# Kernel tuning notes

Measured on AMD Instinct MI355X. Metric: run time of the kernel, lower is better.

Reference implementation:

```python
import jax, jax.numpy as jnp
import numpy as np

N_NODES = 20000
N_EDGES = 640000
HIDDEN = 128
NUM_FILTERS = 128
NUM_RBF = 50
NUM_LAYERS = 6
MAX_Z = 100
CUTOFF_UPPER = 5.0
CUTOFF_LOWER = 0.0


def _cosine_cutoff(d):
    # torchmd CosineCutoff with cutoff_lower == 0
    c = 0.5 * (jnp.cos(d * jnp.pi / CUTOFF_UPPER) + 1.0)
    return c * (d < CUTOFF_UPPER).astype(d.dtype)


def setup_inputs() -> dict:
    key = jax.random.key(0)
    ks = jax.random.split(key, 16)
    s = 0.05
    z = jax.random.randint(ks[0], (N_NODES,), 0, MAX_Z)
    pos = jax.random.uniform(ks[1], (N_NODES, 3), dtype=jnp.float32) * 3.0
    src = jax.random.randint(ks[2], (N_EDGES,), 0, N_NODES)
    off = jax.random.randint(ks[3], (N_EDGES,), 1, N_NODES)
    dst = (src + off) % N_NODES  # no self loops -> d > 0 a.s.
    edge_index = jnp.stack([src, dst])
    batch = jnp.zeros((N_NODES,), dtype=jnp.int32)
    # expnorm RBF initial params (ExpNormalSmearing._initial_params)
    start = float(np.exp(-CUTOFF_UPPER + CUTOFF_LOWER))
    rbf_means = jnp.linspace(start, 1.0, NUM_RBF, dtype=jnp.float32)
    rbf_betas = jnp.full((NUM_RBF,), (2.0 / NUM_RBF * (1.0 - start)) ** -2, dtype=jnp.float32)

    def w(k, shape):
        return jax.random.normal(k, shape, dtype=jnp.float32) * s

    L = NUM_LAYERS
    return dict(
        z=z, pos=pos, edge_index=edge_index, batch=batch,
        emb_table=w(ks[4], (MAX_Z, HIDDEN)),
        nbr_emb_table=w(ks[5], (MAX_Z, HIDDEN)),
        nbr_proj_W=w(ks[6], (NUM_RBF, HIDDEN)),
        nbr_proj_b=jnp.zeros((HIDDEN,), jnp.float32),
        combine_W=w(ks[7], (2 * HIDDEN, HIDDEN)),
        combine_b=jnp.zeros((HIDDEN,), jnp.float32),
        rbf_means=rbf_means, rbf_betas=rbf_betas,
        mlp_W1=w(ks[8], (L, NUM_RBF, NUM_FILTERS)),
        mlp_b1=jnp.zeros((L, NUM_FILTERS), jnp.float32),
        mlp_W2=w(ks[9], (L, NUM_FILTERS, NUM_FILTERS)),
        mlp_b2=jnp.zeros((L, NUM_FILTERS), jnp.float32),
        lin1_W=w(ks[10], (L, HIDDEN, NUM_FILTERS)),
        lin2_W=w(ks[11], (L, NUM_FILTERS, HIDDEN)),
        lin2_b=jnp.zeros((L, HIDDEN), jnp.float32),
        lin_W=w(ks[12], (L, HIDDEN, HIDDEN)),
        lin_b=jnp.zeros((L, HIDDEN), jnp.float32),
    )


def reference(z, pos, edge_index, batch, emb_table, nbr_emb_table,
              nbr_proj_W, nbr_proj_b, combine_W, combine_b,
              rbf_means, rbf_betas,
              mlp_W1, mlp_b1, mlp_W2, mlp_b2,
              lin1_W, lin2_W, lin2_b, lin_W, lin_b):
    src, dst = edge_index[0], edge_index[1]
    # Distance (loop=False): edge_vec = pos[src] - pos[dst]
    vec = pos[src] - pos[dst]                      # [E, 3]
    d = jnp.sqrt(jnp.sum(vec * vec, axis=-1))      # [E]
    C = _cosine_cutoff(d)                          # [E]
    alpha = 5.0 / (CUTOFF_UPPER - CUTOFF_LOWER)
    # ExpNormalSmearing: C(d) * exp(-beta * (exp(alpha*(-d+low)) - mu)^2)
    edge_attr = C[:, None] * jnp.exp(
        -rbf_betas * (jnp.exp(alpha * (-d[:, None] + CUTOFF_LOWER)) - rbf_means) ** 2
    )                                              # [E, R]
    x = emb_table[z]                               # [N, H]
    # NeighborEmbedding (self-loop edges masked out, add aggregation)
    nl_mask = (src != dst).astype(x.dtype)
    Wn = (edge_attr @ nbr_proj_W + nbr_proj_b) * (C * nl_mask)[:, None]  # [E, H]
    xn = nbr_emb_table[z]
    agg = jax.ops.segment_sum(xn[src] * Wn, dst, num_segments=N_NODES)
    x = jnp.concatenate([x, agg], axis=1) @ combine_W + combine_b

    def layer(xc, p):
        W1, b1, W2, b2, l1W, l2W, l2b, lW, lb = p
        # CFConv filter: MLP(edge_attr) * cosine_cutoff
        Wf = (jax.nn.silu(edge_attr @ W1 + b1) @ W2 + b2) * C[:, None]   # [E, F]
        h = xc @ l1W                                                      # [N, F]
        ag = jax.ops.segment_sum(h[src] * Wf, dst, num_segments=N_NODES)  # scatter-add
        h = jax.nn.silu(ag @ l2W + l2b)
        h = h @ lW + lb
        return xc + h, None

    x, _ = jax.lax.scan(layer, x, (mlp_W1, mlp_b1, mlp_W2, mlp_b2,
                                   lin1_W, lin2_W, lin2_b, lin_W, lin_b))
    return x
```

## Files before the change

### kernel.cpp

```cpp
#include <hip/hip_runtime.h>
#include <hip/hip_bf16.h>
#include <math.h>

#define NN 20000
#define NE 640000
#define H  128
#define RB 50
#define NL 6
#define TBINS 4096

typedef unsigned short u16;
typedef __attribute__((ext_vector_type(8))) short short8v;
typedef __attribute__((ext_vector_type(4))) float f32x4;

__device__ __forceinline__ u16 f2b(float v) {
  unsigned x = __float_as_uint(v);
  unsigned r = (x + 0x7FFFu + ((x >> 16) & 1u)) >> 16;
  return (u16)r;
}
__device__ __forceinline__ float b2f(u16 u) {
  return __uint_as_float(((unsigned int)u) << 16);
}

__global__ void k_zero_i32(int* __restrict__ p, int n) {
  int i = blockIdx.x * blockDim.x + threadIdx.x;
  if (i < n) p[i] = 0;
}
__global__ void k_hist(const int* __restrict__ ei, int* __restrict__ counts) {
  int e = blockIdx.x * blockDim.x + threadIdx.x;
  if (e < NE) atomicAdd(&counts[ei[NE + e]], 1);
}
__global__ __launch_bounds__(1024) void k_scan(const int* __restrict__ counts,
                                               int* __restrict__ cursor) {
  __shared__ int tsum[1024];
  int tid = threadIdx.x;
  int base = tid * 20;
  int s = 0;
  #pragma unroll
  for (int j = 0; j < 20; ++j) {
    int i = base + j;
    s += (i < NN) ? counts[i] : 0;
  }
  tsum[tid] = s;
  __syncthreads();
  for (int off = 1; off < 1024; off <<= 1) {
    int t = (tid >= off) ? tsum[tid - off] : 0;
    __syncthreads();
    tsum[tid] += t;
    __syncthreads();
  }
  int run = (tid > 0) ? tsum[tid - 1] : 0;
  #pragma unroll
  for (int j = 0; j < 20; ++j) {
    int i = base + j;
    if (i < NN) { cursor[i] = run; run += counts[i]; }
  }
}
__global__ void k_place(const int* __restrict__ ei, int* __restrict__ cursor,
                        int* __restrict__ perm) {
  int e = blockIdx.x * blockDim.x + threadIdx.x;
  if (e < NE) {
    int d = ei[NE + e];
    int p = atomicAdd(&cursor[d], 1);
    perm[p] = e;
  }
}

__global__ void k_edge(const int* __restrict__ ei, const int* __restrict__ perm,
                       const float* __restrict__ pos,
                       int* __restrict__ srcS, float* __restrict__ tvS) {
  int p = blockIdx.x * 256 + threadIdx.x;
  if (p >= NE) return;
  int e = perm[p];
  int s = ei[e], t = ei[NE + e];
  srcS[p] = s;
  float dx = pos[3*s]   - pos[3*t];
  float dy = pos[3*s+1] - pos[3*t+1];
  float dz = pos[3*s+2] - pos[3*t+2];
  float d = sqrtf(dx*dx + dy*dy + dz*dz);
  tvS[p] = expf(-d);
}

__global__ __launch_bounds__(256) void k_tbuild(
    const float* __restrict__ means, const float* __restrict__ betas,
    const float* __restrict__ npW, const float* __restrict__ npb,
    const float* __restrict__ W1, const float* __restrict__ b1,
    const float* __restrict__ W2, const float* __restrict__ b2,
    u16* __restrict__ tb)
{
  int t  = blockIdx.x / (TBINS / 32);
  int j0 = (blockIdx.x % (TBINS / 32)) * 32;
  __shared__ float sAttr[32][52];
  __shared__ float sCut[32];
  __shared__ float sT[32][132];
  int tid = threadIdx.x;
  float tv0 = expf(-5.f);
  float dtv = (1.f - tv0) / (float)(TBINS - 1);
  for (int idx = tid; idx < 32 * RB; idx += 256) {
    int r = idx / RB, k = idx % RB;
    float tv = tv0 + (j0 + r) * dtv;
    float d = -logf(tv);
    float C = 0.5f * (cosf(d * 0.628318530717958647692f) + 1.f);
    if (d >= 5.f) C = 0.f;
    float diff = tv - means[k];
    sAttr[r][k] = C * expf(-betas[k] * diff * diff);
    if (k == 0) sCut[r] = C;
  }
  __syncthreads();
  int g = tid >> 5, c0 = (tid & 31) * 4, eb = g * 4;
  float acc[4][4];
  #pragma unroll
  for (int i = 0; i < 4; ++i)
    for (int j = 0; j < 4; ++j) acc[i][j] = 0.f;
  const float* Wa = (t == 0) ? npW : (W1 + (size_t)(t - 1) * RB * H);
  for (int k = 0; k < RB; ++k) {
    float4 wv = *(const float4*)&Wa[(size_t)k * H + c0];
    #pragma unroll
    for (int i = 0; i < 4; ++i) {
      float a = sAttr[eb + i][k];
      acc[i][0] += a * wv.x; acc[i][1] += a * wv.y;
      acc[i][2] += a * wv.z; acc[i][3] += a * wv.w;
    }
  }
  size_t obase = (size_t)t * TBINS * H;
  int pb = (c0 & 15) * 8 + (c0 >> 4);
  if (t == 0) {
    float4 b4 = *(const float4*)&npb[c0];
    float bvA[4] = {b4.x, b4.y, b4.z, b4.w};
    #pragma unroll
    for (int i = 0; i < 4; ++i) {
      float Cv = sCut[eb + i];
      size_t rb = obase + (size_t)(j0 + eb + i) * H;
      #pragma unroll
      for (int j = 0; j < 4; ++j)
        tb[rb + pb + 8 * j] = f2b((acc[i][j] + bvA[j]) * Cv);
    }
  } else {
    float4 b4 = *(const float4*)&b1[(size_t)(t - 1) * H + c0];
    float bvA[4] = {b4.x, b4.y, b4.z, b4.w};
    #pragma unroll
    for (int i = 0; i < 4; ++i) {
      #pragma unroll
      for (int j = 0; j < 4; ++j) {
        float v = acc[i][j] + bvA[j];
        sT[eb + i][c0 + j] = v / (1.f + __expf(-v));
      }
    }
    __syncthreads();
    #pragma unroll
    for (int i = 0; i < 4; ++i)
      for (int j = 0; j < 4; ++j) acc[i][j] = 0.f;
    const float* Wb = W2 + (size_t)(t - 1) * H * H;
    for (int k = 0; k < H; ++k) {
      float4 wv = *(const float4*)&Wb[(size_t)k * H + c0];
      #pragma unroll
      for (int i = 0; i < 4; ++i) {
        float a = sT[eb + i][k];
        acc[i][0] += a * wv.x; acc[i][1] += a * wv.y;
        acc[i][2] += a * wv.z; acc[i][3] += a * wv.w;
      }
    }
    float4 b24 = *(const float4*)&b2[(size_t)(t - 1) * H + c0];
    float bvB[4] = {b24.x, b24.y, b24.z, b24.w};
    #pragma unroll
    for (int i = 0; i < 4; ++i) {
      float Cv = sCut[eb + i];
      size_t rb = obase + (size_t)(j0 + eb + i) * H;
      #pragma unroll
      for (int j = 0; j < 4; ++j)
        tb[rb + pb + 8 * j] = f2b((acc[i][j] + bvB[j]) * Cv);
    }
  }
}

#define WBLK (128 * 136)
__global__ void k_prepw2(const float* __restrict__ l2W, const float* __restrict__ lW,
                         const float* __restrict__ l1W, const float* __restrict__ cW,
                         u16* __restrict__ wt) {
  int i = blockIdx.x * 256 + threadIdx.x;
  if (i >= (3 * NL + 2) * WBLK) return;
  if (i < 3 * NL * WBLK) {
    int a = i / (NL * WBLK);
    int r = i % (NL * WBLK);
    int l = r / WBLK;
    int r2 = r % WBLK;
    int n = r2 / 136, k = r2 % 136;
    const float* src = (a == 0) ? l2W : (a == 1) ? lW : l1W;
    wt[i] = (k < H) ? f2b(src[(size_t)l * H * H + (size_t)k * H + n]) : (u16)0;
  } else {
    int j = i - 3 * NL * WBLK;
    int which = j / WBLK;
    int r2 = j % WBLK;
    int n = r2 / 136, k = r2 % 136;
    wt[i] = (k < H) ? f2b(cW[(size_t)(which * 128 + k) * H + n]) : (u16)0;
  }
}

__global__ void k_embed(const int* __restrict__ z, const float* __restrict__ emb,
                        const float* __restrict__ nemb,
                        float* __restrict__ x, u16* __restrict__ xnb) {
  int i = blockIdx.x * blockDim.x + threadIdx.x;
  if (i >= NN * H) return;
  int n = i >> 7, c = i & (H - 1);
  long o = (long)z[n] * H + c;
  x[i] = emb[o];
  xnb[(size_t)n * H + ((c & 15) * 8 + (c >> 4))] = f2b(nemb[o]);
}

__global__ __launch_bounds__(256) void k_eso(
    const int* __restrict__ counts, const int* __restrict__ cursor,
    const int* __restrict__ srcS, const float* __restrict__ tvS,
    const u16* __restrict__ tb, const u16* __restrict__ hsrc,
    float* __restrict__ agg, int maskSelf)
{
  int tid = threadIdx.x;
  int n = blockIdx.x * 16 + (tid >> 4);
  int r16 = tid & 15;
  int cnt = counts[n];
  long e0 = (long)cursor[n] - cnt;
  float tv0 = expf(-5.f);
  float inv = (float)(TBINS - 1) / (1.f - tv0);
  float vsum[8];
  #pragma unroll
  for (int ct = 0; ct < 8; ++ct) vsum[ct] = 0.f;
  int P0_s = 0, P1_s = 0, P2_s = 0;
  float P0_w = 0.f, P1_w = 0.f, P2_w = 0.f;
  short8v P0_hv, P0_lo, P0_hi, P1_hv, P1_lo, P1_hi, P2_hv, P2_lo, P2_hi;
#define ISSUE(P, ii) { int _i = (ii); if (_i < cnt) { \
    long e = e0 + _i; \
    P##_s = srcS[e]; float tvv = tvS[e]; \
    P##_hv = *(const short8v*)&hsrc[(size_t)P##_s * H + r16 * 8]; \
    float u = fminf(fmaxf((tvv - tv0) * inv, 0.f), (float)(TBINS - 1) - 1e-3f); \
    int jj = (int)u; P##_w = u - (float)jj; \
    P##_lo = *(const short8v*)&tb[(size_t)jj * H + r16 * 8]; \
    P##_hi = *(const short8v*)&tb[(size_t)(jj + 1) * H + r16 * 8]; } }
#define CONSUME(P) { \
    float m = (maskSelf && P##_s == n) ? 0.f : 1.f; \
    _Pragma("unroll") \
    for (int ct = 0; ct < 8; ++ct) { \
      float lo = b2f((u16)P##_lo[ct]); \
      float hi = b2f((u16)P##_hi[ct]); \
      vsum[ct] += (lo + P##_w * (hi - lo)) * m * b2f((u16)P##_hv[ct]); \
    } }
  ISSUE(P0, 0); ISSUE(P1, 1); ISSUE(P2, 2);
  for (int i = 0; i < cnt; i += 3) {
    CONSUME(P0); ISSUE(P0, i + 3);
    if (i + 1 < cnt) { CONSUME(P1); ISSUE(P1, i + 4); }
    if (i + 2 < cnt) { CONSUME(P2); ISSUE(P2, i + 5); }
  }
#undef ISSUE
#undef CONSUME
  float* ap = agg + (size_t)n * H + r16;
  #pragma unroll
  for (int ct = 0; ct < 8; ++ct) ap[ct * 16] = vsum[ct];
}

__global__ __launch_bounds__(256) void k_combineM(
    const float* __restrict__ xb, const float* __restrict__ ag,
    const u16* __restrict__ cWt0, const u16* __restrict__ cWt1,
    const float* __restrict__ cb, const u16* __restrict__ l1W0t,
    float* __restrict__ xout, u16* __restrict__ hb)
{
  __shared__ __align__(16) u16 sX[64 * 136];
  __shared__ __align__(16) u16 sG[64 * 136];
  int tid = threadIdx.x;
  int lane = tid & 63, wv = tid >> 6;
  int r16 = lane & 15, g4 = lane >> 4;
  int n0 = blockIdx.x * 64;
  #pragma unroll
  for (int j = 0; j < 8; ++j) {
    int f4 = tid + j * 256;
    int r = f4 >> 5, c4 = f4 & 31;
    int n = n0 + r;
    float4 vx = make_float4(0.f, 0.f, 0.f, 0.f);
    float4 vg = make_float4(0.f, 0.f, 0.f, 0.f);
    if (n < NN) {
      vx = *(const float4*)&xb[(size_t)n * H + c4 * 4];
      vg = *(const float4*)&ag[(size_t)n * H + c4 * 4];
    }
    *(unsigned*)&sX[r * 136 + c4 * 4]     = (unsigned)f2b(vx.x) | ((unsigned)f2b(vx.y) << 16);
    *(unsigned*)&sX[r * 136 + c4 * 4 + 2] = (unsigned)f2b(vx.z) | ((unsigned)f2b(vx.w) << 16);
    *(unsigned*)&sG[r * 136 + c4 * 4]     = (unsigned)f2b(vg.x) | ((unsigned)f2b(vg.y) << 16);
    *(unsigned*)&sG[r * 136 + c4 * 4 + 2] = (unsigned)f2b(vg.z) | ((unsigned)f2b(vg.w) << 16);
  }
  __syncthreads();
  int wrow = wv * 16;
  f32x4 acc[8];
  #pragma unroll
  for (int ct = 0; ct < 8; ++ct) acc[ct] = (f32x4){0.f, 0.f, 0.f, 0.f};
  #pragma unroll
  for (int kt = 0; kt < 4; ++kt) {
    short8v aF = *(const short8v*)&sX[(wrow + r16) * 136 + kt * 32 + g4 * 8];
    #pragma unroll
    for (int ct = 0; ct < 8; ++ct) {
      short8v bF = *(const short8v*)&cWt0[(ct * 16 + r16) * 136 + kt * 32 + g4 * 8];
      acc[ct] = __builtin_amdgcn_mfma_f32_16x16x32_bf16(aF, bF, acc[ct], 0, 0, 0);
    }
  }
  #pragma unroll
  for (int kt = 0; kt < 4; ++kt) {
    short8v aF = *(const short8v*)&sG[(wrow + r16) * 136 + kt * 32 + g4 * 8];
    #pragma unroll
    for (int ct = 0; ct < 8; ++ct) {
      short8v bF = *(const short8v*)&cWt1[(ct * 16 + r16) * 136 + kt * 32 + g4 * 8];
      acc[ct] = __builtin_amdgcn_mfma_f32_16x16x32_bf16(aF, bF, acc[ct], 0, 0, 0);
    }
  }
  #pragma unroll
  for (int ct = 0; ct < 8; ++ct) {
    float bb = cb[ct * 16 + r16];
    #pragma unroll
    for (int r = 0; r < 4; ++r) {
      int n = n0 + wrow + g4 * 4 + r;
      if (n < NN) {
        float o = acc[ct][r] + bb;
        xout[(size_t)n * H + ct * 16 + r16] = o;
        sX[(wrow + g4 * 4 + r) * 136 + ct * 16 + r16] = f2b(o);
      }
    }
  }
  #pragma unroll
  for (int ct = 0; ct < 8; ++ct) acc[ct] = (f32x4){0.f, 0.f, 0.f, 0.f};
  #pragma unroll
  for (int kt = 0; kt < 4; ++kt) {
    short8v aF = *(const short8v*)&sX[(wrow + r16) * 136 + kt * 32 + g4 * 8];
    #pragma unroll
    for (int ct = 0; ct < 8; ++ct) {
      short8v bF = *(const short8v*)&l1W0t[(ct * 16 + r16) * 136 + kt * 32 + g4 * 8];
      acc[ct] = __builtin_amdgcn_mfma_f32_16x16x32_bf16(aF, bF, acc[ct], 0, 0, 0);
    }
  }
  #pragma unroll
  for (int r = 0; r < 4; ++r) {
    int n = n0 + wrow + g4 * 4 + r;
    if (n < NN) {
      short8v hv;
      #pragma unroll
      for (int ct = 0; ct < 8; ++ct) hv[ct] = (short)f2b(acc[ct][r]);
      *(short8v*)&hb[(size_t)n * H + r16 * 8] = hv;
    }
  }
}

__global__ __launch_bounds__(256) void k_gemmM(
    const float* __restrict__ A, const u16* __restrict__ W2t, const float* __restrict__ b2,
    const u16* __restrict__ W3t, const float* __restrict__ b3,
    const float* __restrict__ xin, float* __restrict__ xout,
    const u16* __restrict__ l1Wnt, u16* __restrict__ hb)
{
  __shared__ __align__(16) u16 sA[64 * 136];
  __shared__ __align__(16) u16 sT[64 * 136];
  int tid = threadIdx.x;
  int lane = tid & 63, wv = tid >> 6;
  int r16 = lane & 15, g4 = lane >> 4;
  int n0 = blockIdx.x * 64;
  #pragma unroll
  for (int j = 0; j < 8; ++j) {
    int f4 = tid + j * 256;
    int r = f4 >> 5, c4 = f4 & 31;
    int n = n0 + r;
    float4 v = make_float4(0.f, 0.f, 0.f, 0.f);
    if (n < NN) v = *(const float4*)&A[(size_t)n * H + c4 * 4];
    *(unsigned*)&sA[r * 136 + c4 * 4]     = (unsigned)f2b(v.x) | ((unsigned)f2b(v.y) << 16);
    *(unsigned*)&sA[r * 136 + c4 * 4 + 2] = (unsigned)f2b(v.z) | ((unsigned)f2b(v.w) << 16);
  }
  __syncthreads();
  int wrow = wv * 16;
  f32x4 acc[8];
  #pragma unroll
  for (int ct = 0; ct < 8; ++ct) acc[ct] = (f32x4){0.f, 0.f, 0.f, 0.f};
  #pragma unroll
  for (int kt = 0; kt < 4; ++kt) {
    short8v aF = *(const short8v*)&sA[(wrow + r16) * 136 + kt * 32 + g4 * 8];
    #pragma unroll
    for (int ct = 0; ct < 8; ++ct) {
      short8v bF = *(const short8v*)&W2t[(ct * 16 + r16) * 136 + kt * 32 + g4 * 8];
      acc[ct] = __builtin_amdgcn_mfma_f32_16x16x32_bf16(aF, bF, acc[ct], 0, 0, 0);
    }
  }
  #pragma unroll
  for (int ct = 0; ct < 8; ++ct) {
    float bb = b2[ct * 16 + r16];
    #pragma unroll
    for (int r = 0; r < 4; ++r) {
      float v = acc[ct][r] + bb;
      v = v / (1.f + __expf(-v));
      sT[(wrow + g4 * 4 + r) * 136 + ct * 16 + r16] = f2b(v);
    }
  }
  #pragma unroll
  for (int ct = 0; ct < 8; ++ct) acc[ct] = (f32x4){0.f, 0.f, 0.f, 0.f};
  #pragma unroll
  for (int kt = 0; kt < 4; ++kt) {
    short8v aF = *(const short8v*)&sT[(wrow + r16) * 136 + kt * 32 + g4 * 8];
    #pragma unroll
    for (int ct = 0; ct < 8; ++ct) {
      short8v bF = *(const short8v*)&W3t[(ct * 16 + r16) * 136 + kt * 32 + g4 * 8];
      acc[ct] = __builtin_amdgcn_mfma_f32_16x16x32_bf16(aF, bF, acc[ct], 0, 0, 0);
    }
  }
  #pragma unroll
  for (int ct = 0; ct < 8; ++ct) {
    float bb = b3[ct * 16 + r16];
    #pragma unroll
    for (int r = 0; r < 4; ++r) {
      int n = n0 + wrow + g4 * 4 + r;
      if (n < NN) {
        float o = acc[ct][r] + bb + xin[(size_t)n * H + ct * 16 + r16];
        xout[(size_t)n * H + ct * 16 + r16] = o;
        sA[(wrow + g4 * 4 + r) * 136 + ct * 16 + r16] = f2b(o);
      }
    }
  }
  if (!l1Wnt) return;
  #pragma unroll
  for (int ct = 0; ct < 8; ++ct) acc[ct] = (f32x4){0.f, 0.f, 0.f, 0.f};
  #pragma unroll
  for (int kt = 0; kt < 4; ++kt) {
    short8v aF = *(const short8v*)&sA[(wrow + r16) * 136 + kt * 32 + g4 * 8];
    #pragma unroll
    for (int ct = 0; ct < 8; ++ct) {
      short8v bF = *(const short8v*)&l1Wnt[(ct * 16 + r16) * 136 + kt * 32 + g4 * 8];
      acc[ct] = __builtin_amdgcn_mfma_f32_16x16x32_bf16(aF, bF, acc[ct], 0, 0, 0);
    }
  }
  #pragma unroll
  for (int r = 0; r < 4; ++r) {
    int n = n0 + wrow + g4 * 4 + r;
    if (n < NN) {
      short8v hv;
      #pragma unroll
      for (int ct = 0; ct < 8; ++ct) hv[ct] = (short)f2b(acc[ct][r]);
      *(short8v*)&hb[(size_t)n * H + r16 * 8] = hv;
    }
  }
}

extern "C" void kernel_launch(void* const* d_in, const int* in_sizes, int n_in,
                              void* d_out, int out_size, void* d_ws, size_t ws_size,
                              hipStream_t stream) {
  int bo = (n_in >= 4 && in_sizes[3] == NN) ? 0 : -1;
  const int*   z     = (const int*)d_in[0];
  const float* pos   = (const float*)d_in[1];
  const int*   ei    = (const int*)d_in[2];
  const float* emb   = (const float*)d_in[4 + bo];
  const float* nemb  = (const float*)d_in[5 + bo];
  const float* npW   = (const float*)d_in[6 + bo];
  const float* npb   = (const float*)d_in[7 + bo];
  const float* cW    = (const float*)d_in[8 + bo];
  const float* cb    = (const float*)d_in[9 + bo];
  const float* means = (const float*)d_in[10 + bo];
  const float* betas = (const float*)d_in[11 + bo];
  const float* W1    = (const float*)d_in[12 + bo];
  const float* b1    = (const float*)d_in[13 + bo];
  const float* W2    = (const float*)d_in[14 + bo];
  const float* b2    = (const float*)d_in[15 + bo];
  const float* l1W   = (const float*)d_in[16 + bo];
  const float* l2W   = (const float*)d_in[17 + bo];
  const float* l2b   = (const float*)d_in[18 + bo];
  const float* lW    = (const float*)d_in[19 + bo];
  const float* lb    = (const float*)d_in[20 + bo];

  char* w = (char*)d_ws;
  auto alloc = [&](size_t bytes) { char* p = w; w += (bytes + 255) & ~(size_t)255; return p; };
  int*   counts = (int*)  alloc((size_t)NN * 4);
  int*   cursor = (int*)  alloc((size_t)NN * 4);
  int*   perm   = (int*)  alloc((size_t)NE * 4);
  int*   srcS   = (int*)  alloc((size_t)NE * 4);
  float* tvS    = (float*)alloc((size_t)NE * 4);
  u16*   tb     = (u16*)  alloc((size_t)7 * TBINS * H * 2);
  u16*   wt     = (u16*)  alloc((size_t)(3 * NL + 2) * WBLK * 2);
  float* xbuf   = (float*)alloc((size_t)NN * H * 4);
  float* agg    = (float*)alloc((size_t)NN * H * 4);
  u16*   xnb    = (u16*)  alloc((size_t)NN * H * 2);
  u16*   hbuf   = (u16*)  alloc((size_t)NN * H * 2);

  u16* l2Wt = wt;
  u16* lWt  = wt + (size_t)NL * WBLK;
  u16* l1Wt = wt + (size_t)2 * NL * WBLK;
  u16* cWt0 = wt + (size_t)3 * NL * WBLK;
  u16* cWt1 = cWt0 + WBLK;

  dim3 b256(256);
  int gE256 = (NE + 255) / 256;
  int gNH   = (NN * H + 255) / 256;
  int gESO  = NN / 16;
  int gM    = (NN + 63) / 64;
  int gTB   = 7 * (TBINS / 32);
  int gPW   = ((3 * NL + 2) * WBLK + 255) / 256;

  k_zero_i32<<<(NN + 255) / 256, b256, 0, stream>>>(counts, NN);
  k_hist<<<gE256, b256, 0, stream>>>(ei, counts);
  k_scan<<<1, 1024, 0, stream>>>(counts, cursor);
  k_place<<<gE256, b256, 0, stream>>>(ei, cursor, perm);
  k_edge<<<gE256, b256, 0, stream>>>(ei, perm, pos, srcS, tvS);
  k_tbuild<<<gTB, b256, 0, stream>>>(means, betas, npW, npb, W1, b1, W2, b2, tb);
  k_prepw2<<<gPW, b256, 0, stream>>>(l2W, lW, l1W, cW, wt);
  k_embed<<<gNH, b256, 0, stream>>>(z, emb, nemb, xbuf, xnb);

  k_eso<<<gESO, b256, 0, stream>>>(counts, cursor, srcS, tvS, tb, xnb, agg, 1);
  k_combineM<<<gM, b256, 0, stream>>>(xbuf, agg, cWt0, cWt1, cb, l1Wt, xbuf, hbuf);

  for (int l = 0; l < NL; ++l) {
    k_eso<<<gESO, b256, 0, stream>>>(counts, cursor, srcS, tvS,
                                     tb + (size_t)(1 + l) * TBINS * H,
                                     hbuf, agg, 0);
    const u16* l1Wnt = (l + 1 < NL) ? (l1Wt + (size_t)(l + 1) * WBLK) : nullptr;
    float* xo = (l == NL - 1) ? (float*)d_out : xbuf;
    k_gemmM<<<gM, b256, 0, stream>>>(agg, l2Wt + (size_t)l * WBLK, l2b + (size_t)l * H,
                                     lWt + (size_t)l * WBLK, lb + (size_t)l * H,
                                     xbuf, xo, l1Wnt, hbuf);
  }
}
```

Baseline: 674.9 us.

## Fuse edge gather-aggregation into per-layer node GEMM kernels with ping-pong h buffers

The separate edge aggregation kernel is merged into the node MLP kernels, for both the embedding-combine stage and every interaction layer. Each 64-node block now walks its own nodes' edges, writing bf16 aggregates straight into shared memory. This removes the fp32 agg buffer's global write and read-back, plus one launch per layer. Because other blocks may still be reading h while a block writes the next layer's h, h now alternates between two buffers. The cost is much less gather parallelism: about 313 blocks, with each 16-thread group walking 4 nodes one after another, which may hurt latency hiding in the memory-bound gather.

Result: slower. 1.001 ms (+48.3%).

```diff
diff --git a/kernel.cpp b/kernel.cpp
--- a/kernel.cpp
+++ b/kernel.cpp
@@ -8,6 +8,7 @@
 #define RB 50
 #define NL 6
 #define TBINS 4096
+#define WBLK (128 * 136)
 
 typedef unsigned short u16;
 typedef __attribute__((ext_vector_type(8))) short short8v;
@@ -173,7 +174,6 @@
   }
 }
 
-#define WBLK (128 * 136)
 __global__ void k_prepw2(const float* __restrict__ l2W, const float* __restrict__ lW,
                          const float* __restrict__ l1W, const float* __restrict__ cW,
                          u16* __restrict__ wt) {
@@ -207,22 +207,17 @@
   xnb[(size_t)n * H + ((c & 15) * 8 + (c >> 4))] = f2b(nemb[o]);
 }
 
-__global__ __launch_bounds__(256) void k_eso(
-    const int* __restrict__ counts, const int* __restrict__ cursor,
+__device__ __forceinline__ void edge_walk(
+    int n, int r16, const int* __restrict__ counts, const int* __restrict__ cursor,
     const int* __restrict__ srcS, const float* __restrict__ tvS,
     const u16* __restrict__ tb, const u16* __restrict__ hsrc,
-    float* __restrict__ agg, int maskSelf)
+    int maskSelf, float tv0, float inv, float vsum[8])
 {
-  int tid = threadIdx.x;
-  int n = blockIdx.x * 16 + (tid >> 4);
-  int r16 = tid & 15;
+  #pragma unroll
+  for (int ct = 0; ct < 8; ++ct) vsum[ct] = 0.f;
+  if (n >= NN) return;
   int cnt = counts[n];
   long e0 = (long)cursor[n] - cnt;
-  float tv0 = expf(-5.f);
-  float inv = (float)(TBINS - 1) / (1.f - tv0);
-  float vsum[8];
-  #pragma unroll
-  for (int ct = 0; ct < 8; ++ct) vsum[ct] = 0.f;
   int P0_s = 0, P1_s = 0, P2_s = 0;
   float P0_w = 0.f, P1_w = 0.f, P2_w = 0.f;
   short8v P0_hv, P0_lo, P0_hi, P1_hv, P1_lo, P1_hi, P2_hv, P2_lo, P2_hi;
@@ -250,13 +245,112 @@
   }
 #undef ISSUE
 #undef CONSUME
-  float* ap = agg + (size_t)n * H + r16;
-  #pragma unroll
-  for (int ct = 0; ct < 8; ++ct) ap[ct * 16] = vsum[ct];
-}
-
-__global__ __launch_bounds__(256) void k_combineM(
-    const float* __restrict__ xb, const float* __restrict__ ag,
+}
+
+__global__ __launch_bounds__(256) void k_fused(
+    const int* __restrict__ counts, const int* __restrict__ cursor,
+    const int* __restrict__ srcS, const float* __restrict__ tvS,
+    const u16* __restrict__ tb, const u16* __restrict__ hsrc,
+    const u16* __restrict__ W2t, const float* __restrict__ b2,
+    const u16* __restrict__ W3t, const float* __restrict__ b3,
+    const float* __restrict__ xin, float* __restrict__ xout,
+    const u16* __restrict__ l1Wnt, u16* __restrict__ hb)
+{
+  __shared__ __align__(16) u16 sA[64 * 136];
+  __shared__ __align__(16) u16 sT[64 * 136];
+  int tid = threadIdx.x;
+  int grp = tid >> 4, r16g = tid & 15;
+  int n0 = blockIdx.x * 64;
+  float tv0 = expf(-5.f);
+  float inv = (float)(TBINS - 1) / (1.f - tv0);
+  for (int q = 0; q < 4; ++q) {
+    int row = grp * 4 + q;
+    int n = n0 + row;
+    float vsum[8];
+    edge_walk(n, r16g, counts, cursor, srcS, tvS, tb, hsrc, 0, tv0, inv, vsum);
+    #pragma unroll
+    for (int ct = 0; ct < 8; ++ct)
+      sA[row * 136 + ct * 16 + r16g] = f2b(vsum[ct]);
+  }
+  __syncthreads();
+  int lane = tid & 63, wv = tid >> 6;
+  int r16 = lane & 15, g4 = lane >> 4;
+  int wrow = wv * 16;
+  f32x4 acc[8];
+  #pragma unroll
+  for (int ct = 0; ct < 8; ++ct) acc[ct] = (f32x4){0.f, 0.f, 0.f, 0.f};
+  #pragma unroll
+  for (int kt = 0; kt < 4; ++kt) {
+    short8v aF = *(const short8v*)&sA[(wrow + r16) * 136 + kt * 32 + g4 * 8];
+    #pragma unroll
+    for (int ct = 0; ct < 8; ++ct) {
+      short8v bF = *(const short8v*)&W2t[(ct * 16 + r16) * 136 + kt * 32 + g4 * 8];
+      acc[ct] = __builtin_amdgcn_mfma_f32_16x16x32_bf16(aF, bF, acc[ct], 0, 0, 0);
+    }
+  }
+  #pragma unroll
+  for (int ct = 0; ct < 8; ++ct) {
+    float bb = b2[ct * 16 + r16];
+    #pragma unroll
+    for (int r = 0; r < 4; ++r) {
+      float v = acc[ct][r] + bb;
+      v = v / (1.f + __expf(-v));
+      sT[(wrow + g4 * 4 + r) * 136 + ct * 16 + r16] = f2b(v);
+    }
+  }
+  #pragma unroll
+  for (int ct = 0; ct < 8; ++ct) acc[ct] = (f32x4){0.f, 0.f, 0.f, 0.f};
+  #pragma unroll
+  for (int kt = 0; kt < 4; ++kt) {
+    short8v aF = *(const short8v*)&sT[(wrow + r16) * 136 + kt * 32 + g4 * 8];
+    #pragma unroll
+    for (int ct = 0; ct < 8; ++ct) {
+      short8v bF = *(const short8v*)&W3t[(ct * 16 + r16) * 136 + kt * 32 + g4 * 8];
+      acc[ct] = __builtin_amdgcn_mfma_f32_16x16x32_bf16(aF, bF, acc[ct], 0, 0, 0);
+    }
+  }
+  #pragma unroll
+  for (int ct = 0; ct < 8; ++ct) {
+    float bb = b3[ct * 16 + r16];
+    #pragma unroll
+    for (int r = 0; r < 4; ++r) {
+      int n = n0 + wrow + g4 * 4 + r;
+      if (n < NN) {
+        float o = acc[ct][r] + bb + xin[(size_t)n * H + ct * 16 + r16];
+        xout[(size_t)n * H + ct * 16 + r16] = o;
+        sA[(wrow + g4 * 4 + r) * 136 + ct * 16 + r16] = f2b(o);
+      }
+    }
+  }
+  if (!l1Wnt) return;
+  #pragma unroll
+  for (int ct = 0; ct < 8; ++ct) acc[ct] = (f32x4){0.f, 0.f, 0.f, 0.f};
+  #pragma unroll
+  for (int kt = 0; kt < 4; ++kt) {
+    short8v aF = *(const short8v*)&sA[(wrow + r16) * 136 + kt * 32 + g4 * 8];
+    #pragma unroll
+    for (int ct = 0; ct < 8; ++ct) {
+      short8v bF = *(const short8v*)&l1Wnt[(ct * 16 + r16) * 136 + kt * 32 + g4 * 8];
+      acc[ct] = __builtin_amdgcn_mfma_f32_16x16x32_bf16(aF, bF, acc[ct], 0, 0, 0);
+    }
+  }
+  #pragma unroll
+  for (int r = 0; r < 4; ++r) {
+    int n = n0 + wrow + g4 * 4 + r;
+    if (n < NN) {
+      short8v hv;
+      #pragma unroll
+      for (int ct = 0; ct < 8; ++ct) hv[ct] = (short)f2b(acc[ct][r]);
+      *(short8v*)&hb[(size_t)n * H + r16 * 8] = hv;
+    }
+  }
+}
+
+__global__ __launch_bounds__(256) void k_fusedC(
+    const int* __restrict__ counts, const int* __restrict__ cursor,
+    const int* __restrict__ srcS, const float* __restrict__ tvS,
+    const u16* __restrict__ tb, const u16* __restrict__ xnb,
+    const float* __restrict__ xb,
     const u16* __restrict__ cWt0, const u16* __restrict__ cWt1,
     const float* __restrict__ cb, const u16* __restrict__ l1W0t,
     float* __restrict__ xout, u16* __restrict__ hb)
@@ -264,26 +358,32 @@
   __shared__ __align__(16) u16 sX[64 * 136];
   __shared__ __align__(16) u16 sG[64 * 136];
   int tid = threadIdx.x;
-  int lane = tid & 63, wv = tid >> 6;
-  int r16 = lane & 15, g4 = lane >> 4;
+  int grp = tid >> 4, r16g = tid & 15;
   int n0 = blockIdx.x * 64;
+  float tv0 = expf(-5.f);
+  float inv = (float)(TBINS - 1) / (1.f - tv0);
   #pragma unroll
   for (int j = 0; j < 8; ++j) {
     int f4 = tid + j * 256;
     int r = f4 >> 5, c4 = f4 & 31;
     int n = n0 + r;
-    float4 vx = make_float4(0.f, 0.f, 0.f, 0.f);
-    float4 vg = make_float4(0.f, 0.f, 0.f, 0.f);
-    if (n < NN) {
-      vx = *(const float4*)&xb[(size_t)n * H + c4 * 4];
-      vg = *(const float4*)&ag[(size_t)n * H + c4 * 4];
-    }
-    *(unsigned*)&sX[r * 136 + c4 * 4]     = (unsigned)f2b(vx.x) | ((unsigned)f2b(vx.y) << 16);
-    *(unsigned*)&sX[r * 136 + c4 * 4 + 2] = (unsigned)f2b(vx.z) | ((unsigned)f2b(vx.w) << 16);
-    *(unsigned*)&sG[r * 136 + c4 * 4]     = (unsigned)f2b(vg.x) | ((unsigned)f2b(vg.y) << 16);
-    *(unsigned*)&sG[r * 136 + c4 * 4 + 2] = (unsigned)f2b(vg.z) | ((unsigned)f2b(vg.w) << 16);
+    float4 v = make_float4(0.f, 0.f, 0.f, 0.f);
+    if (n < NN) v = *(const float4*)&xb[(size_t)n * H + c4 * 4];
+    *(unsigned*)&sX[r * 136 + c4 * 4]     = (unsigned)f2b(v.x) | ((unsigned)f2b(v.y) << 16);
+    *(unsigned*)&sX[r * 136 + c4 * 4 + 2] = (unsigned)f2b(v.z) | ((unsigned)f2b(v.w) << 16);
+  }
+  for (int q = 0; q < 4; ++q) {
+    int row = grp * 4 + q;
+    int n = n0 + row;
+    float vsum[8];
+    edge_walk(n, r16g, counts, cursor, srcS, tvS, tb, xnb, 1, tv0, inv, vsum);
+    #pragma unroll
+    for (int ct = 0; ct < 8; ++ct)
+      sG[row * 136 + ct * 16 + r16g] = f2b(vsum[ct]);
   }
   __syncthreads();
+  int lane = tid & 63, wv = tid >> 6;
+  int r16 = lane & 15, g4 = lane >> 4;
   int wrow = wv * 16;
   f32x4 acc[8];
   #pragma unroll
@@ -306,6 +406,7 @@
       acc[ct] = __builtin_amdgcn_mfma_f32_16x16x32_bf16(aF, bF, acc[ct], 0, 0, 0);
     }
   }
+  __syncthreads();
   #pragma unroll
   for (int ct = 0; ct < 8; ++ct) {
     float bb = cb[ct * 16 + r16];
@@ -327,100 +428,6 @@
     #pragma unroll
     for (int ct = 0; ct < 8; ++ct) {
       short8v bF = *(const short8v*)&l1W0t[(ct * 16 + r16) * 136 + kt * 32 + g4 * 8];
-      acc[ct] = __builtin_amdgcn_mfma_f32_16x16x32_bf16(aF, bF, acc[ct], 0, 0, 0);
-    }
-  }
-  #pragma unroll
-  for (int r = 0; r < 4; ++r) {
-    int n = n0 + wrow + g4 * 4 + r;
-    if (n < NN) {
-      short8v hv;
-      #pragma unroll
-      for (int ct = 0; ct < 8; ++ct) hv[ct] = (short)f2b(acc[ct][r]);
-      *(short8v*)&hb[(size_t)n * H + r16 * 8] = hv;
-    }
-  }
-}
-
-__global__ __launch_bounds__(256) void k_gemmM(
-    const float* __restrict__ A, const u16* __restrict__ W2t, const float* __restrict__ b2,
-    const u16* __restrict__ W3t, const float* __restrict__ b3,
-    const float* __restrict__ xin, float* __restrict__ xout,
-    const u16* __restrict__ l1Wnt, u16* __restrict__ hb)
-{
-  __shared__ __align__(16) u16 sA[64 * 136];
-  __shared__ __align__(16) u16 sT[64 * 136];
-  int tid = threadIdx.x;
-  int lane = tid & 63, wv = tid >> 6;
-  int r16 = lane & 15, g4 = lane >> 4;
-  int n0 = blockIdx.x * 64;
-  #pragma unroll
-  for (int j = 0; j < 8; ++j) {
-    int f4 = tid + j * 256;
-    int r = f4 >> 5, c4 = f4 & 31;
-    int n = n0 + r;
-    float4 v = make_float4(0.f, 0.f, 0.f, 0.f);
-    if (n < NN) v = *(const float4*)&A[(size_t)n * H + c4 * 4];
-    *(unsigned*)&sA[r * 136 + c4 * 4]     = (unsigned)f2b(v.x) | ((unsigned)f2b(v.y) << 16);
-    *(unsigned*)&sA[r * 136 + c4 * 4 + 2] = (unsigned)f2b(v.z) | ((unsigned)f2b(v.w) << 16);
-  }
-  __syncthreads();
-  int wrow = wv * 16;
-  f32x4 acc[8];
-  #pragma unroll
-  for (int ct = 0; ct < 8; ++ct) acc[ct] = (f32x4){0.f, 0.f, 0.f, 0.f};
-  #pragma unroll
-  for (int kt = 0; kt < 4; ++kt) {
-    short8v aF = *(const short8v*)&sA[(wrow + r16) * 136 + kt * 32 + g4 * 8];
-    #pragma unroll
-    for (int ct = 0; ct < 8; ++ct) {
-      short8v bF = *(const short8v*)&W2t[(ct * 16 + r16) * 136 + kt * 32 + g4 * 8];
-      acc[ct] = __builtin_amdgcn_mfma_f32_16x16x32_bf16(aF, bF, acc[ct], 0, 0, 0);
-    }
-  }
-  #pragma unroll
-  for (int ct = 0; ct < 8; ++ct) {
-    float bb = b2[ct * 16 + r16];
-    #pragma unroll
-    for (int r = 0; r < 4; ++r) {
-      float v = acc[ct][r] + bb;
-      v = v / (1.f + __expf(-v));
-      sT[(wrow + g4 * 4 + r) * 136 + ct * 16 + r16] = f2b(v);
-    }
-  }
-  #pragma unroll
-  for (int ct = 0; ct < 8; ++ct) acc[ct] = (f32x4){0.f, 0.f, 0.f, 0.f};
-  #pragma unroll
-  for (int kt = 0; kt < 4; ++kt) {
-    short8v aF = *(const short8v*)&sT[(wrow + r16) * 136 + kt * 32 + g4 * 8];
-    #pragma unroll
-    for (int ct = 0; ct < 8; ++ct) {
-      short8v bF = *(const short8v*)&W3t[(ct * 16 + r16) * 136 + kt * 32 + g4 * 8];
-      acc[ct] = __builtin_amdgcn_mfma_f32_16x16x32_bf16(aF, bF, acc[ct], 0, 0, 0);
-    }
-  }
-  #pragma unroll
-  for (int ct = 0; ct < 8; ++ct) {
-    float bb = b3[ct * 16 + r16];
-    #pragma unroll
-    for (int r = 0; r < 4; ++r) {
-      int n = n0 + wrow + g4 * 4 + r;
-      if (n < NN) {
-        float o = acc[ct][r] + bb + xin[(size_t)n * H + ct * 16 + r16];
-        xout[(size_t)n * H + ct * 16 + r16] = o;
-        sA[(wrow + g4 * 4 + r) * 136 + ct * 16 + r16] = f2b(o);
-      }
-    }
-  }
-  if (!l1Wnt) return;
-  #pragma unroll
-  for (int ct = 0; ct < 8; ++ct) acc[ct] = (f32x4){0.f, 0.f, 0.f, 0.f};
-  #pragma unroll
-  for (int kt = 0; kt < 4; ++kt) {
-    short8v aF = *(const short8v*)&sA[(wrow + r16) * 136 + kt * 32 + g4 * 8];
-    #pragma unroll
-    for (int ct = 0; ct < 8; ++ct) {
-      short8v bF = *(const short8v*)&l1Wnt[(ct * 16 + r16) * 136 + kt * 32 + g4 * 8];
       acc[ct] = __builtin_amdgcn_mfma_f32_16x16x32_bf16(aF, bF, acc[ct], 0, 0, 0);
     }
   }
@@ -471,9 +478,9 @@
   u16*   tb     = (u16*)  alloc((size_t)7 * TBINS * H * 2);
   u16*   wt     = (u16*)  alloc((size_t)(3 * NL + 2) * WBLK * 2);
   float* xbuf   = (float*)alloc((size_t)NN * H * 4);
-  float* agg    = (float*)alloc((size_t)NN * H * 4);
   u16*   xnb    = (u16*)  alloc((size_t)NN * H * 2);
-  u16*   hbuf   = (u16*)  alloc((size_t)NN * H * 2);
+  u16*   hbA    = (u16*)  alloc((size_t)NN * H * 2);
+  u16*   hbB    = (u16*)  alloc((size_t)NN * H * 2);
 
   u16* l2Wt = wt;
   u16* lWt  = wt + (size_t)NL * WBLK;
@@ -484,7 +491,6 @@
   dim3 b256(256);
   int gE256 = (NE + 255) / 256;
   int gNH   = (NN * H + 255) / 256;
-  int gESO  = NN / 16;
   int gM    = (NN + 63) / 64;
   int gTB   = 7 * (TBINS / 32);
   int gPW   = ((3 * NL + 2) * WBLK + 255) / 256;
@@ -498,17 +504,19 @@
   k_prepw2<<<gPW, b256, 0, stream>>>(l2W, lW, l1W, cW, wt);
   k_embed<<<gNH, b256, 0, stream>>>(z, emb, nemb, xbuf, xnb);
 
-  k_eso<<<gESO, b256, 0, stream>>>(counts, cursor, srcS, tvS, tb, xnb, agg, 1);
-  k_combineM<<<gM, b256, 0, stream>>>(xbuf, agg, cWt0, cWt1, cb, l1Wt, xbuf, hbuf);
-
+  k_fusedC<<<gM, b256, 0, stream>>>(counts, cursor, srcS, tvS, tb, xnb, xbuf,
+                                    cWt0, cWt1, cb, l1Wt, xbuf, hbA);
+
+  u16* hin = hbA;
+  u16* hout = hbB;
   for (int l = 0; l < NL; ++l) {
-    k_eso<<<gESO, b256, 0, stream>>>(counts, cursor, srcS, tvS,
-                                     tb + (size_t)(1 + l) * TBINS * H,
-                                     hbuf, agg, 0);
     const u16* l1Wnt = (l + 1 < NL) ? (l1Wt + (size_t)(l + 1) * WBLK) : nullptr;
     float* xo = (l == NL - 1) ? (float*)d_out : xbuf;
-    k_gemmM<<<gM, b256, 0, stream>>>(agg, l2Wt + (size_t)l * WBLK, l2b + (size_t)l * H,
+    k_fused<<<gM, b256, 0, stream>>>(counts, cursor, srcS, tvS,
+                                     tb + (size_t)(1 + l) * TBINS * H, hin,
+                                     l2Wt + (size_t)l * WBLK, l2b + (size_t)l * H,
                                      lWt + (size_t)l * WBLK, lb + (size_t)l * H,
-                                     xbuf, xo, l1Wnt, hbuf);
-  }
-}
+                                     xbuf, xo, l1Wnt, hout);
+    u16* tmp = hin; hin = hout; hout = tmp;
+  }
+}
```

## Process two nodes per lane group in edge aggregation and halve GEMM block tiles

Applied to the files above, without the earlier changes.

The edge-gather kernel now has each 16-lane group handle two destination nodes with interleaved prefetch streams, which doubles the loads in flight per thread to hide gather latency. The node GEMM kernel uses 32-row tiles with 128 threads, giving twice as many blocks to spread across CUs. Bounds checks are dropped because NN divides evenly. The zeroing kernel becomes a hipMemsetAsync, and the h buffer is double-buffered between layers. The trade-off is higher register pressure in the gather kernel and more divergence when the two nodes' degrees differ.

Result: slower. 734.9 us (+8.9%).

```diff
diff --git a/kernel.cpp b/kernel.cpp
--- a/kernel.cpp
+++ b/kernel.cpp
@@ -8,6 +8,7 @@
 #define RB 50
 #define NL 6
 #define TBINS 4096
+#define WBLK (128 * 136)
 
 typedef unsigned short u16;
 typedef __attribute__((ext_vector_type(8))) short short8v;
@@ -22,10 +23,6 @@
   return __uint_as_float(((unsigned int)u) << 16);
 }
 
-__global__ void k_zero_i32(int* __restrict__ p, int n) {
-  int i = blockIdx.x * blockDim.x + threadIdx.x;
-  if (i < n) p[i] = 0;
-}
 __global__ void k_hist(const int* __restrict__ ei, int* __restrict__ counts) {
   int e = blockIdx.x * blockDim.x + threadIdx.x;
   if (e < NE) atomicAdd(&counts[ei[NE + e]], 1);
@@ -173,7 +170,6 @@
   }
 }
 
-#define WBLK (128 * 136)
 __global__ void k_prepw2(const float* __restrict__ l2W, const float* __restrict__ lW,
                          const float* __restrict__ l1W, const float* __restrict__ cW,
                          u16* __restrict__ wt) {
@@ -214,19 +210,20 @@
     float* __restrict__ agg, int maskSelf)
 {
   int tid = threadIdx.x;
-  int n = blockIdx.x * 16 + (tid >> 4);
-  int r16 = tid & 15;
-  int cnt = counts[n];
-  long e0 = (long)cursor[n] - cnt;
+  int grp = tid >> 4, r16 = tid & 15;
+  int nA = blockIdx.x * 32 + grp * 2;
+  int nB = nA + 1;
+  int cntA = counts[nA], cntB = counts[nB];
+  long e0A = (long)cursor[nA] - cntA;
+  long e0B = (long)cursor[nB] - cntB;
   float tv0 = expf(-5.f);
   float inv = (float)(TBINS - 1) / (1.f - tv0);
-  float vsum[8];
-  #pragma unroll
-  for (int ct = 0; ct < 8; ++ct) vsum[ct] = 0.f;
-  int P0_s = 0, P1_s = 0, P2_s = 0;
-  float P0_w = 0.f, P1_w = 0.f, P2_w = 0.f;
-  short8v P0_hv, P0_lo, P0_hi, P1_hv, P1_lo, P1_hi, P2_hv, P2_lo, P2_hi;
-#define ISSUE(P, ii) { int _i = (ii); if (_i < cnt) { \
+  float vsA[8], vsB[8];
+  #pragma unroll
+  for (int ct = 0; ct < 8; ++ct) { vsA[ct] = 0.f; vsB[ct] = 0.f; }
+#define DECLS(P) int P##_s = 0; float P##_w = 0.f; short8v P##_hv, P##_lo, P##_hi;
+  DECLS(A0) DECLS(A1) DECLS(A2) DECLS(B0) DECLS(B1) DECLS(B2)
+#define ISSUE(P, e0, cnt, ii) { int _i = (ii); if (_i < cnt) { \
     long e = e0 + _i; \
     P##_s = srcS[e]; float tvv = tvS[e]; \
     P##_hv = *(const short8v*)&hsrc[(size_t)P##_s * H + r16 * 8]; \
@@ -234,25 +231,33 @@
     int jj = (int)u; P##_w = u - (float)jj; \
     P##_lo = *(const short8v*)&tb[(size_t)jj * H + r16 * 8]; \
     P##_hi = *(const short8v*)&tb[(size_t)(jj + 1) * H + r16 * 8]; } }
-#define CONSUME(P) { \
-    float m = (maskSelf && P##_s == n) ? 0.f : 1.f; \
+#define CONSUME(P, nd, vs) { \
+    float m = (maskSelf && P##_s == nd) ? 0.f : 1.f; \
     _Pragma("unroll") \
     for (int ct = 0; ct < 8; ++ct) { \
       float lo = b2f((u16)P##_lo[ct]); \
       float hi = b2f((u16)P##_hi[ct]); \
-      vsum[ct] += (lo + P##_w * (hi - lo)) * m * b2f((u16)P##_hv[ct]); \
+      vs[ct] += (lo + P##_w * (hi - lo)) * m * b2f((u16)P##_hv[ct]); \
     } }
-  ISSUE(P0, 0); ISSUE(P1, 1); ISSUE(P2, 2);
-  for (int i = 0; i < cnt; i += 3) {
-    CONSUME(P0); ISSUE(P0, i + 3);
-    if (i + 1 < cnt) { CONSUME(P1); ISSUE(P1, i + 4); }
-    if (i + 2 < cnt) { CONSUME(P2); ISSUE(P2, i + 5); }
+  ISSUE(A0, e0A, cntA, 0); ISSUE(B0, e0B, cntB, 0);
+  ISSUE(A1, e0A, cntA, 1); ISSUE(B1, e0B, cntB, 1);
+  ISSUE(A2, e0A, cntA, 2); ISSUE(B2, e0B, cntB, 2);
+  int mx = max(cntA, cntB);
+  for (int i = 0; i < mx; i += 3) {
+    if (i < cntA) { CONSUME(A0, nA, vsA); ISSUE(A0, e0A, cntA, i + 3); }
+    if (i < cntB) { CONSUME(B0, nB, vsB); ISSUE(B0, e0B, cntB, i + 3); }
+    if (i + 1 < cntA) { CONSUME(A1, nA, vsA); ISSUE(A1, e0A, cntA, i + 4); }
+    if (i + 1 < cntB) { CONSUME(B1, nB, vsB); ISSUE(B1, e0B, cntB, i + 4); }
+    if (i + 2 < cntA) { CONSUME(A2, nA, vsA); ISSUE(A2, e0A, cntA, i + 5); }
+    if (i + 2 < cntB) { CONSUME(B2, nB, vsB); ISSUE(B2, e0B, cntB, i + 5); }
   }
 #undef ISSUE
 #undef CONSUME
-  float* ap = agg + (size_t)n * H + r16;
-  #pragma unroll
-  for (int ct = 0; ct < 8; ++ct) ap[ct * 16] = vsum[ct];
+#undef DECLS
+  float* apA = agg + (size_t)nA * H + r16;
+  float* apB = agg + (size_t)nB * H + r16;
+  #pragma unroll
+  for (int ct = 0; ct < 8; ++ct) { apA[ct * 16] = vsA[ct]; apB[ct * 16] = vsB[ct]; }
 }
 
 __global__ __launch_bounds__(256) void k_combineM(
@@ -342,25 +347,23 @@
   }
 }
 
-__global__ __launch_bounds__(256) void k_gemmM(
+__global__ __launch_bounds__(128) void k_gemmM(
     const float* __restrict__ A, const u16* __restrict__ W2t, const float* __restrict__ b2,
     const u16* __restrict__ W3t, const float* __restrict__ b3,
     const float* __restrict__ xin, float* __restrict__ xout,
     const u16* __restrict__ l1Wnt, u16* __restrict__ hb)
 {
-  __shared__ __align__(16) u16 sA[64 * 136];
-  __shared__ __align__(16) u16 sT[64 * 136];
+  __shared__ __align__(16) u16 sA[32 * 136];
+  __shared__ __align__(16) u16 sT[32 * 136];
   int tid = threadIdx.x;
   int lane = tid & 63, wv = tid >> 6;
   int r16 = lane & 15, g4 = lane >> 4;
-  int n0 = blockIdx.x * 64;
+  int n0 = blockIdx.x * 32;
   #pragma unroll
   for (int j = 0; j < 8; ++j) {
-    int f4 = tid + j * 256;
+    int f4 = tid + j * 128;
     int r = f4 >> 5, c4 = f4 & 31;
-    int n = n0 + r;
-    float4 v = make_float4(0.f, 0.f, 0.f, 0.f);
-    if (n < NN) v = *(const float4*)&A[(size_t)n * H + c4 * 4];
+    float4 v = *(const float4*)&A[(size_t)(n0 + r) * H + c4 * 4];
     *(unsigned*)&sA[r * 136 + c4 * 4]     = (unsigned)f2b(v.x) | ((unsigned)f2b(v.y) << 16);
     *(unsigned*)&sA[r * 136 + c4 * 4 + 2] = (unsigned)f2b(v.z) | ((unsigned)f2b(v.w) << 16);
   }
@@ -405,11 +408,9 @@
     #pragma unroll
     for (int r = 0; r < 4; ++r) {
       int n = n0 + wrow + g4 * 4 + r;
-      if (n < NN) {
-        float o = acc[ct][r] + bb + xin[(size_t)n * H + ct * 16 + r16];
-        xout[(size_t)n * H + ct * 16 + r16] = o;
-        sA[(wrow + g4 * 4 + r) * 136 + ct * 16 + r16] = f2b(o);
-      }
+      float o = acc[ct][r] + bb + xin[(size_t)n * H + ct * 16 + r16];
+      xout[(size_t)n * H + ct * 16 + r16] = o;
+      sA[(wrow + g4 * 4 + r) * 136 + ct * 16 + r16] = f2b(o);
     }
   }
   if (!l1Wnt) return;
@@ -427,12 +428,10 @@
   #pragma unroll
   for (int r = 0; r < 4; ++r) {
     int n = n0 + wrow + g4 * 4 + r;
-    if (n < NN) {
-      short8v hv;
-      #pragma unroll
-      for (int ct = 0; ct < 8; ++ct) hv[ct] = (short)f2b(acc[ct][r]);
-      *(short8v*)&hb[(size_t)n * H + r16 * 8] = hv;
-    }
+    short8v hv;
+    #pragma unroll
+    for (int ct = 0; ct < 8; ++ct) hv[ct] = (short)f2b(acc[ct][r]);
+    *(short8v*)&hb[(size_t)n * H + r16 * 8] = hv;
   }
 }
 
@@ -473,7 +472,8 @@
   float* xbuf   = (float*)alloc((size_t)NN * H * 4);
   float* agg    = (float*)alloc((size_t)NN * H * 4);
   u16*   xnb    = (u16*)  alloc((size_t)NN * H * 2);
-  u16*   hbuf   = (u16*)  alloc((size_t)NN * H * 2);
+  u16*   hbA    = (u16*)  alloc((size_t)NN * H * 2);
+  u16*   hbB    = (u16*)  alloc((size_t)NN * H * 2);
 
   u16* l2Wt = wt;
   u16* lWt  = wt + (size_t)NL * WBLK;
@@ -484,12 +484,13 @@
   dim3 b256(256);
   int gE256 = (NE + 255) / 256;
   int gNH   = (NN * H + 255) / 256;
-  int gESO  = NN / 16;
-  int gM    = (NN + 63) / 64;
+  int gESO  = NN / 32;
+  int gC    = (NN + 63) / 64;
+  int gM    = NN / 32;
   int gTB   = 7 * (TBINS / 32);
   int gPW   = ((3 * NL + 2) * WBLK + 255) / 256;
 
-  k_zero_i32<<<(NN + 255) / 256, b256, 0, stream>>>(counts, NN);
+  hipMemsetAsync(counts, 0, (size_t)NN * 4, stream);
   k_hist<<<gE256, b256, 0, stream>>>(ei, counts);
   k_scan<<<1, 1024, 0, stream>>>(counts, cursor);
   k_place<<<gE256, b256, 0, stream>>>(ei, cursor, perm);
@@ -499,16 +500,19 @@
   k_embed<<<gNH, b256, 0, stream>>>(z, emb, nemb, xbuf, xnb);
 
   k_eso<<<gESO, b256, 0, stream>>>(counts, cursor, srcS, tvS, tb, xnb, agg, 1);
-  k_combineM<<<gM, b256, 0, stream>>>(xbuf, agg, cWt0, cWt1, cb, l1Wt, xbuf, hbuf);
-
+  k_combineM<<<gC, b256, 0, stream>>>(xbuf, agg, cWt0, cWt1, cb, l1Wt, xbuf, hbA);
+
+  u16* hin = hbA;
+  u16* hout = hbB;
   for (int l = 0; l < NL; ++l) {
     k_eso<<<gESO, b256, 0, stream>>>(counts, cursor, srcS, tvS,
                                      tb + (size_t)(1 + l) * TBINS * H,
-                                     hbuf, agg, 0);
+                                     hin, agg, 0);
     const u16* l1Wnt = (l + 1 < NL) ? (l1Wt + (size_t)(l + 1) * WBLK) : nullptr;
     float* xo = (l == NL - 1) ? (float*)d_out : xbuf;
-    k_gemmM<<<gM, b256, 0, stream>>>(agg, l2Wt + (size_t)l * WBLK, l2b + (size_t)l * H,
-                                     lWt + (size_t)l * WBLK, lb + (size_t)l * H,
-                                     xbuf, xo, l1Wnt, hbuf);
-  }
-}
+    k_gemmM<<<gM, dim3(128), 0, stream>>>(agg, l2Wt + (size_t)l * WBLK, l2b + (size_t)l * H,
+                                          lWt + (size_t)l * WBLK, lb + (size_t)l * H,
+                                          xbuf, xo, l1Wnt, hout);
+    u16* tmp = hin; hin = hout; hout = tmp;
+  }
+}
```
